# Performance work log

Hardware: AMD Instinct MI355X
Metric: run time of the kernel (lower is better)

Reference implementation:

```python
import jax, jax.numpy as jnp
import numpy as np
import math

B, S_MAX, D = 16, 4096, 4096
H, H_KV, D_H = 32, 8, 128
REP = H // H_KV
START_POS = S_MAX - 1  # decode at last slot -> attend over full cache


def _rope(t, cos, sin):
    # t: [B, 1, h, D_H]; cos/sin: [1, D_H//2] (per-position rotary factors)
    b, s, h, dh = t.shape
    tr = t.reshape(b, s, h, dh // 2, 2)
    e, o = tr[..., 0], tr[..., 1]          # even / odd components
    c = cos[None, :, None, :]              # [1, 1, 1, D_H//2]
    sn = sin[None, :, None, :]
    out = jnp.stack([e * c - o * sn, e * sn + o * c], axis=-1)
    return out.reshape(b, s, h, dh)


def setup_inputs() -> dict:
    key = jax.random.key(0)
    ks = jax.random.split(key, 8)
    x = jax.random.normal(ks[0], (B, 1, D), dtype=jnp.float32)
    cache_k = jax.random.normal(ks[1], (B, S_MAX, H_KV, D_H), dtype=jnp.float32) * 0.02
    cache_v = jax.random.normal(ks[2], (B, S_MAX, H_KV, D_H), dtype=jnp.float32) * 0.02
    wq = jax.random.normal(ks[3], (D, H * D_H), dtype=jnp.float32) * 0.02
    wk = jax.random.normal(ks[4], (D, H_KV * D_H), dtype=jnp.float32) * 0.02
    wv = jax.random.normal(ks[5], (D, H_KV * D_H), dtype=jnp.float32) * 0.02
    wo = jax.random.normal(ks[6], (H * D_H, D), dtype=jnp.float32) * 0.02
    # real RoPE angles for position START_POS
    inv_freq = 1.0 / (10000.0 ** (np.arange(0, D_H, 2, dtype=np.float32) / D_H))
    ang = np.float32(START_POS) * inv_freq  # [D_H//2]
    freqs_cos = jnp.asarray(np.cos(ang))[None, :]  # [1, 64]
    freqs_sin = jnp.asarray(np.sin(ang))[None, :]
    return {"x": x, "cache_k": cache_k, "cache_v": cache_v,
            "wq": wq, "wk": wk, "wv": wv, "wo": wo,
            "freqs_cos": freqs_cos, "freqs_sin": freqs_sin,
            "start_pos": START_POS}


def reference(x, cache_k, cache_v, wq, wk, wv, wo, freqs_cos, freqs_sin, start_pos):
    b = x.shape[0]
    xq = (x @ wq).reshape(b, 1, H, D_H)
    xk = (x @ wk).reshape(b, 1, H_KV, D_H)
    xv = (x @ wv).reshape(b, 1, H_KV, D_H)
    xq = _rope(xq, freqs_cos, freqs_sin)
    xk = _rope(xk, freqs_cos, freqs_sin)
    # KV-cache append (start_pos is a Python int -> static slice)
    cache_k = jax.lax.dynamic_update_slice(cache_k, xk, (0, start_pos, 0, 0))
    cache_v = jax.lax.dynamic_update_slice(cache_v, xv, (0, start_pos, 0, 0))
    L = start_pos + 1
    keys = cache_k[:, :L]    # [B, L, H_KV, D_H]
    # NOTE: original has `values = repeat_kv(keys, num_rep)` -- values == keys (bug),
    # reproduced faithfully here. cache_v is still written, matching the original.
    q = xq.reshape(b, 1, H_KV, REP, D_H)
    # GQA scores without materializing the repeated KV tensor
    scores = jnp.einsum('bqkrd,bskd->bkrqs', q, keys) / math.sqrt(D_H)
    attn = jax.nn.softmax(scores, axis=-1)
    out = jnp.einsum('bkrqs,bskd->bqkrd', attn, keys)  # values == keys (faithful bug)
    out = out.reshape(b, 1, H * D_H) @ wo
    return out
```

## Files before the change

kernel.cpp:

```cpp
#include <hip/hip_runtime.h>
#include <math.h>

#define BATCH 16
#define SMAX 4096
#define DMODEL 4096
#define NH 32
#define NKV 8
#define NREP 4
#define DH 128
#define QKCOLS 5120
#define NCHUNK 8
#define CHUNK 512
#define TILE 64

__global__ __launch_bounds__(256) void gemv_part(
    const float* __restrict__ in,
    const float* __restrict__ w1, int c1,
    const float* __restrict__ w2, int c2,
    float* __restrict__ part)
{
    const int tile = blockIdx.x;
    const int ch = blockIdx.y;
    const int t = threadIdx.x;
    const int col = tile * 256 + t;
    const int totC = c1 + c2;
    const int d0 = ch * 256;

    __shared__ float xs[BATCH * 256];
    for (int b = 0; b < BATCH; ++b)
        xs[b * 256 + t] = in[(size_t)b * DMODEL + d0 + t];
    __syncthreads();

    const float* w; int stride, wcol;
    if (col < c1) { w = w1; stride = c1; wcol = col; }
    else          { w = w2; stride = c2; wcol = col - c1; }

    float acc[BATCH];
#pragma unroll
    for (int b = 0; b < BATCH; ++b) acc[b] = 0.f;

    const float* wp = w + (size_t)d0 * stride + wcol;
    for (int d = 0; d < 256; d += 4) {
        float wa = wp[(size_t)(d + 0) * stride];
        float wb = wp[(size_t)(d + 1) * stride];
        float wc = wp[(size_t)(d + 2) * stride];
        float wd = wp[(size_t)(d + 3) * stride];
#pragma unroll
        for (int b = 0; b < BATCH; ++b) {
            const float4 xv = *(const float4*)&xs[b * 256 + d];
            float a = acc[b];
            a = fmaf(xv.x, wa, a);
            a = fmaf(xv.y, wb, a);
            a = fmaf(xv.z, wc, a);
            a = fmaf(xv.w, wd, a);
            acc[b] = a;
        }
    }
#pragma unroll
    for (int b = 0; b < BATCH; ++b)
        part[((size_t)ch * BATCH + b) * totC + col] = acc[b];
}

__global__ __launch_bounds__(256) void rope_reduce(
    const float* __restrict__ part,
    const float* __restrict__ fcos, const float* __restrict__ fsin,
    float* __restrict__ xqk)
{
    int g = blockIdx.x * 256 + threadIdx.x;
    int b = g / 2560;
    int po = g % 2560;
    float e = 0.f, o = 0.f;
    const float* p = part + (size_t)b * QKCOLS + 2 * po;
#pragma unroll
    for (int ch = 0; ch < 16; ++ch) {
        float2 v = *(const float2*)(p + (size_t)ch * BATCH * QKCOLS);
        e += v.x; o += v.y;
    }
    int i = po & 63;
    float c = fcos[i], s = fsin[i];
    xqk[(size_t)b * QKCOLS + 2 * po]     = e * c - o * s;
    xqk[(size_t)b * QKCOLS + 2 * po + 1] = e * s + o * c;
}

__global__ __launch_bounds__(256) void attn_part_kernel(
    const float* __restrict__ cache_k,
    const float* __restrict__ xqk,
    const int* __restrict__ sp,
    float* __restrict__ out)
{
    const int chunk = blockIdx.x;
    const int kv = blockIdx.y;
    const int b = blockIdx.z;
    const int t = threadIdx.x;
    const int dl = t & 63;
    const int r = t >> 6;
    const int start_pos = sp[0];

    __shared__ float k_lds[TILE * DH];

    const int h = kv * NREP + r;
    const float* qp = xqk + (size_t)b * QKCOLS + h * DH;
    const int half = dl & 31;
    const int hi = dl >> 5;
    float4 q4 = *(const float4*)(qp + half * 4);
    const float scale = 0.08838834764831845f;
    q4.x *= scale; q4.y *= scale; q4.z *= scale; q4.w *= scale;
    const int row_owned = (half << 1) + hi;

    const float* xknew = xqk + (size_t)b * QKCOLS + DMODEL + kv * DH;
    const float* kbase = cache_k + ((size_t)b * SMAX * NKV + kv) * DH;

    float m_run = -1e30f, l_run = 0.f;
    float2 acc = make_float2(0.f, 0.f);

    for (int tt = 0; tt < CHUNK / TILE; ++tt) {
        const int s_base = chunk * CHUNK + tt * TILE;
#pragma unroll
        for (int it = 0; it < 8; ++it) {
            int f = it * 256 + t;
            int row = f >> 5;
            int c4 = (f & 31) * 4;
            int s = s_base + row;
            const float* src = (s == start_pos) ? (xknew + c4)
                             : (kbase + (size_t)s * (NKV * DH) + c4);
            *(float4*)&k_lds[row * DH + c4] = *(const float4*)src;
        }
        __syncthreads();

        float score_mine = -1e30f;
        for (int jp = 0; jp < 32; ++jp) {
            int row = 2 * jp + hi;
            const float4 k4 = *(const float4*)&k_lds[row * DH + half * 4];
            float partial = q4.x * k4.x + q4.y * k4.y + q4.z * k4.z + q4.w * k4.w;
#pragma unroll
            for (int m = 1; m < 32; m <<= 1)
                partial += __shfl_xor(partial, m, 64);
            if (half == jp) score_mine = partial;
        }
        if (s_base + row_owned > start_pos) score_mine = -1e30f;

        float m_tile = score_mine;
#pragma unroll
        for (int m = 1; m < 64; m <<= 1)
            m_tile = fmaxf(m_tile, __shfl_xor(m_tile, m, 64));
        float m_new = fmaxf(m_run, m_tile);
        float alpha = __expf(m_run - m_new);
        float p_mine = __expf(score_mine - m_new);
        float psum = p_mine;
#pragma unroll
        for (int m = 1; m < 64; m <<= 1)
            psum += __shfl_xor(psum, m, 64);
        l_run = l_run * alpha + psum;
        acc.x *= alpha; acc.y *= alpha;
        m_run = m_new;

        for (int j = 0; j < 64; ++j) {
            int src_lane = (j >> 1) + ((j & 1) << 5);
            float pj = __shfl(p_mine, src_lane, 64);
            const float2 kj = *(const float2*)&k_lds[j * DH + 2 * dl];
            acc.x = fmaf(pj, kj.x, acc.x);
            acc.y = fmaf(pj, kj.y, acc.y);
        }
        __syncthreads();
    }

    float* rec = out + ((((size_t)b * NKV + kv) * NCHUNK + chunk) * NREP + r) * 130;
    rec[2 * dl] = acc.x;
    rec[2 * dl + 1] = acc.y;
    if (dl == 0) { rec[128] = m_run; rec[129] = l_run; }
}

__global__ __launch_bounds__(128) void attn_combine(
    const float* __restrict__ part, float* __restrict__ attn_out)
{
    const int hq = blockIdx.x;
    const int b = blockIdx.y;
    const int kv = hq >> 2, r = hq & 3;
    const int d = threadIdx.x;
    float m_c[NCHUNK], l_c[NCHUNK];
    float M = -1e30f;
#pragma unroll
    for (int c = 0; c < NCHUNK; ++c) {
        const float* rec = part + ((((size_t)b * NKV + kv) * NCHUNK + c) * NREP + r) * 130;
        m_c[c] = rec[128]; l_c[c] = rec[129];
        M = fmaxf(M, m_c[c]);
    }
    float num = 0.f, den = 0.f;
#pragma unroll
    for (int c = 0; c < NCHUNK; ++c) {
        const float* rec = part + ((((size_t)b * NKV + kv) * NCHUNK + c) * NREP + r) * 130;
        float w = __expf(m_c[c] - M);
        num = fmaf(w, rec[d], num);
        den = fmaf(w, l_c[c], den);
    }
    attn_out[(size_t)b * DMODEL + hq * DH + d] = num / den;
}

__global__ __launch_bounds__(256) void reduce_out(
    const float* __restrict__ part, float* __restrict__ out)
{
    int g = blockIdx.x * 256 + threadIdx.x;
    int b = g >> 12, o = g & 4095;
    float s = 0.f;
#pragma unroll
    for (int ch = 0; ch < 16; ++ch)
        s += part[((size_t)ch * BATCH + b) * DMODEL + o];
    out[g] = s;
}

extern "C" void kernel_launch(void* const* d_in, const int* in_sizes, int n_in,
                              void* d_out, int out_size, void* d_ws, size_t ws_size,
                              hipStream_t stream) {
    const float* x       = (const float*)d_in[0];
    const float* cache_k = (const float*)d_in[1];
    const float* wq      = (const float*)d_in[3];
    const float* wk      = (const float*)d_in[4];
    const float* wo      = (const float*)d_in[6];
    const float* fcos    = (const float*)d_in[7];
    const float* fsin    = (const float*)d_in[8];
    const int*   sp      = (const int*)d_in[9];
    float* out = (float*)d_out;
    float* ws  = (float*)d_ws;

    float* part_qk   = ws;
    float* xqk       = part_qk + 1310720;
    float* attn_part = xqk + 81920;
    float* attn_out  = attn_part + 532480;
    float* part_out  = part_qk;

    gemv_part<<<dim3(QKCOLS / 256, 16), 256, 0, stream>>>(x, wq, 4096, wk, 1024, part_qk);
    rope_reduce<<<160, 256, 0, stream>>>(part_qk, fcos, fsin, xqk);
    attn_part_kernel<<<dim3(NCHUNK, NKV, BATCH), 256, 0, stream>>>(cache_k, xqk, sp, attn_part);
    attn_combine<<<dim3(NH, BATCH), 128, 0, stream>>>(attn_part, attn_out);
    gemv_part<<<dim3(DMODEL / 256, 16), 256, 0, stream>>>(attn_out, wo, 4096, nullptr, 0, part_out);
    reduce_out<<<256, 256, 0, stream>>>(part_out, out);
}
```

Baseline: 733.2 us.

## Rework GEMV split-K and attention kernel with prefetch, swizzled LDS, per-row scores

The GEMV now has each thread own two columns via float2 loads, reads x straight from global memory instead of LDS, and splits K into 64 chunks of 64 rows for more blocks. The reductions are adjusted to match, and the workspace grows. The attention kernel is rewritten so each lane computes one full key-row score from Q held in LDS, which replaces the cross-lane shuffle reduction. It also prefetches the next K tile into registers while computing the current one, uses an XOR-swizzled LDS layout to avoid bank conflicts, and passes probabilities through LDS. The trade-off is more partial-sum traffic in the GEMV reductions, plus higher register pressure and extra barriers in attention.

```diff
diff --git a/kernel.cpp b/kernel.cpp
--- a/kernel.cpp
+++ b/kernel.cpp
@@ -12,6 +12,8 @@
 #define NCHUNK 8
 #define CHUNK 512
 #define TILE 64
+#define NCH 64
+#define GD 64
 
 __global__ __launch_bounds__(256) void gemv_part(
     const float* __restrict__ in,
@@ -19,46 +21,34 @@
     const float* __restrict__ w2, int c2,
     float* __restrict__ part)
 {
-    const int tile = blockIdx.x;
-    const int ch = blockIdx.y;
     const int t = threadIdx.x;
-    const int col = tile * 256 + t;
+    const int col = blockIdx.x * 512 + t * 2;
     const int totC = c1 + c2;
-    const int d0 = ch * 256;
-
-    __shared__ float xs[BATCH * 256];
+    const int d0 = blockIdx.y * GD;
+
+    const float* w; int stride, wc;
+    if (col < c1) { w = w1; stride = c1; wc = col; }
+    else          { w = w2; stride = c2; wc = col - c1; }
+    const float* wp = w + (size_t)d0 * stride + wc;
+
+    float2 acc[BATCH];
+#pragma unroll
+    for (int b = 0; b < BATCH; ++b) acc[b] = make_float2(0.f, 0.f);
+
+#pragma unroll 4
+    for (int i = 0; i < GD; ++i) {
+        const float2 wv = *(const float2*)(wp + (size_t)i * stride);
+#pragma unroll
+        for (int b = 0; b < BATCH; ++b) {
+            const float xv = in[(size_t)b * DMODEL + d0 + i];
+            acc[b].x = fmaf(wv.x, xv, acc[b].x);
+            acc[b].y = fmaf(wv.y, xv, acc[b].y);
+        }
+    }
+    const size_t base = (size_t)blockIdx.y * BATCH;
+#pragma unroll
     for (int b = 0; b < BATCH; ++b)
-        xs[b * 256 + t] = in[(size_t)b * DMODEL + d0 + t];
-    __syncthreads();
-
-    const float* w; int stride, wcol;
-    if (col < c1) { w = w1; stride = c1; wcol = col; }
-    else          { w = w2; stride = c2; wcol = col - c1; }
-
-    float acc[BATCH];
-#pragma unroll
-    for (int b = 0; b < BATCH; ++b) acc[b] = 0.f;
-
-    const float* wp = w + (size_t)d0 * stride + wcol;
-    for (int d = 0; d < 256; d += 4) {
-        float wa = wp[(size_t)(d + 0) * stride];
-        float wb = wp[(size_t)(d + 1) * stride];
-        float wc = wp[(size_t)(d + 2) * stride];
-        float wd = wp[(size_t)(d + 3) * stride];
-#pragma unroll
-        for (int b = 0; b < BATCH; ++b) {
-            const float4 xv = *(const float4*)&xs[b * 256 + d];
-            float a = acc[b];
-            a = fmaf(xv.x, wa, a);
-            a = fmaf(xv.y, wb, a);
-            a = fmaf(xv.z, wc, a);
-            a = fmaf(xv.w, wd, a);
-            acc[b] = a;
-        }
-    }
-#pragma unroll
-    for (int b = 0; b < BATCH; ++b)
-        part[((size_t)ch * BATCH + b) * totC + col] = acc[b];
+        *(float2*)&part[(base + b) * totC + col] = acc[b];
 }
 
 __global__ __launch_bounds__(256) void rope_reduce(
@@ -71,8 +61,8 @@
     int po = g % 2560;
     float e = 0.f, o = 0.f;
     const float* p = part + (size_t)b * QKCOLS + 2 * po;
-#pragma unroll
-    for (int ch = 0; ch < 16; ++ch) {
+#pragma unroll 8
+    for (int ch = 0; ch < NCH; ++ch) {
         float2 v = *(const float2*)(p + (size_t)ch * BATCH * QKCOLS);
         e += v.x; o += v.y;
     }
@@ -82,7 +72,7 @@
     xqk[(size_t)b * QKCOLS + 2 * po + 1] = e * s + o * c;
 }
 
-__global__ __launch_bounds__(256) void attn_part_kernel(
+__global__ __launch_bounds__(256, 4) void attn_part_kernel(
     const float* __restrict__ cache_k,
     const float* __restrict__ xqk,
     const int* __restrict__ sp,
@@ -97,77 +87,123 @@
     const int start_pos = sp[0];
 
     __shared__ float k_lds[TILE * DH];
-
-    const int h = kv * NREP + r;
-    const float* qp = xqk + (size_t)b * QKCOLS + h * DH;
-    const int half = dl & 31;
-    const int hi = dl >> 5;
-    float4 q4 = *(const float4*)(qp + half * 4);
-    const float scale = 0.08838834764831845f;
-    q4.x *= scale; q4.y *= scale; q4.z *= scale; q4.w *= scale;
-    const int row_owned = (half << 1) + hi;
+    __shared__ float q_lds[NREP * DH];
+    __shared__ float p_lds[NREP * TILE];
 
     const float* xknew = xqk + (size_t)b * QKCOLS + DMODEL + kv * DH;
     const float* kbase = cache_k + ((size_t)b * SMAX * NKV + kv) * DH;
+    const float scale = 0.08838834764831845f;
+
+    {
+        const float* qp0 = xqk + (size_t)b * QKCOLS + (kv * NREP) * DH;
+        q_lds[t]       = qp0[t] * scale;
+        q_lds[256 + t] = qp0[256 + t] * scale;
+    }
+
+    float4 st[8];
+
+#define STAGE(TT) do {                                                        \
+        const int s_b_ = chunk * CHUNK + (TT) * TILE;                         \
+        _Pragma("unroll")                                                     \
+        for (int it = 0; it < 8; ++it) {                                      \
+            int f_ = it * 256 + t;                                            \
+            int row_ = f_ >> 5;                                               \
+            int c4_ = f_ & 31;                                                \
+            int s_ = s_b_ + row_;                                             \
+            const float* src_ = (s_ == start_pos) ? (xknew + 4 * c4_)         \
+                              : (kbase + (size_t)s_ * (NKV * DH) + 4 * c4_);  \
+            st[it] = *(const float4*)src_;                                    \
+        }                                                                     \
+    } while (0)
+
+#define KWRITE() do {                                                         \
+        _Pragma("unroll")                                                     \
+        for (int it = 0; it < 8; ++it) {                                      \
+            int f_ = it * 256 + t;                                            \
+            int row_ = f_ >> 5;                                               \
+            int c4_ = f_ & 31;                                                \
+            *(float4*)&k_lds[row_ * DH + ((c4_ ^ (row_ & 7)) << 2)] = st[it]; \
+        }                                                                     \
+    } while (0)
+
+    STAGE(0);
+    KWRITE();
+    __syncthreads();
 
     float m_run = -1e30f, l_run = 0.f;
-    float2 acc = make_float2(0.f, 0.f);
+    float ax = 0.f, ay = 0.f;
+    const float* qh = q_lds + r * DH;
+    const float* krow = k_lds + dl * DH;
+    const int sw = dl & 7;
+    const int c4o = dl >> 1;
+    const int o2 = (2 * dl) & 3;
 
     for (int tt = 0; tt < CHUNK / TILE; ++tt) {
+        if (tt < CHUNK / TILE - 1) STAGE(tt + 1);
+
         const int s_base = chunk * CHUNK + tt * TILE;
-#pragma unroll
-        for (int it = 0; it < 8; ++it) {
-            int f = it * 256 + t;
-            int row = f >> 5;
-            int c4 = (f & 31) * 4;
-            int s = s_base + row;
-            const float* src = (s == start_pos) ? (xknew + c4)
-                             : (kbase + (size_t)s * (NKV * DH) + c4);
-            *(float4*)&k_lds[row * DH + c4] = *(const float4*)src;
-        }
-        __syncthreads();
-
-        float score_mine = -1e30f;
-        for (int jp = 0; jp < 32; ++jp) {
-            int row = 2 * jp + hi;
-            const float4 k4 = *(const float4*)&k_lds[row * DH + half * 4];
-            float partial = q4.x * k4.x + q4.y * k4.y + q4.z * k4.z + q4.w * k4.w;
-#pragma unroll
-            for (int m = 1; m < 32; m <<= 1)
-                partial += __shfl_xor(partial, m, 64);
-            if (half == jp) score_mine = partial;
-        }
-        if (s_base + row_owned > start_pos) score_mine = -1e30f;
-
-        float m_tile = score_mine;
+
+        float c0 = 0.f, c1 = 0.f, c2 = 0.f, c3 = 0.f;
+#pragma unroll 4
+        for (int i = 0; i < 32; ++i) {
+            const float4 q4 = *(const float4*)(qh + 4 * i);
+            const float4 k4 = *(const float4*)(krow + ((i ^ sw) << 2));
+            c0 = fmaf(q4.x, k4.x, c0);
+            c1 = fmaf(q4.y, k4.y, c1);
+            c2 = fmaf(q4.z, k4.z, c2);
+            c3 = fmaf(q4.w, k4.w, c3);
+        }
+        float score = (c0 + c1) + (c2 + c3);
+        if (s_base + dl > start_pos) score = -1e30f;
+
+        float m_tile = score;
 #pragma unroll
         for (int m = 1; m < 64; m <<= 1)
             m_tile = fmaxf(m_tile, __shfl_xor(m_tile, m, 64));
         float m_new = fmaxf(m_run, m_tile);
         float alpha = __expf(m_run - m_new);
-        float p_mine = __expf(score_mine - m_new);
-        float psum = p_mine;
+        float p = __expf(score - m_new);
+        float psum = p;
 #pragma unroll
         for (int m = 1; m < 64; m <<= 1)
             psum += __shfl_xor(psum, m, 64);
         l_run = l_run * alpha + psum;
-        acc.x *= alpha; acc.y *= alpha;
+        ax *= alpha; ay *= alpha;
         m_run = m_new;
 
-        for (int j = 0; j < 64; ++j) {
-            int src_lane = (j >> 1) + ((j & 1) << 5);
-            float pj = __shfl(p_mine, src_lane, 64);
-            const float2 kj = *(const float2*)&k_lds[j * DH + 2 * dl];
-            acc.x = fmaf(pj, kj.x, acc.x);
-            acc.y = fmaf(pj, kj.y, acc.y);
-        }
+        p_lds[r * TILE + dl] = p;
         __syncthreads();
+
+#pragma unroll 4
+        for (int j4 = 0; j4 < 16; ++j4) {
+            const float4 pj = *(const float4*)&p_lds[r * TILE + 4 * j4];
+#define PVROW(JJ, PV) do {                                                    \
+            const int rw_ = 4 * j4 + (JJ);                                    \
+            const float2 k2_ = *(const float2*)&k_lds[rw_ * DH +              \
+                                   ((c4o ^ (rw_ & 7)) << 2) + o2];            \
+            ax = fmaf((PV), k2_.x, ax);                                       \
+            ay = fmaf((PV), k2_.y, ay);                                       \
+        } while (0)
+            PVROW(0, pj.x);
+            PVROW(1, pj.y);
+            PVROW(2, pj.z);
+            PVROW(3, pj.w);
+#undef PVROW
+        }
+        __syncthreads();
+
+        if (tt < CHUNK / TILE - 1) {
+            KWRITE();
+            __syncthreads();
+        }
     }
 
     float* rec = out + ((((size_t)b * NKV + kv) * NCHUNK + chunk) * NREP + r) * 130;
-    rec[2 * dl] = acc.x;
-    rec[2 * dl + 1] = acc.y;
+    rec[2 * dl] = ax;
+    rec[2 * dl + 1] = ay;
     if (dl == 0) { rec[128] = m_run; rec[129] = l_run; }
+#undef STAGE
+#undef KWRITE
 }
 
 __global__ __launch_bounds__(128) void attn_combine(
@@ -202,8 +238,8 @@
     int g = blockIdx.x * 256 + threadIdx.x;
     int b = g >> 12, o = g & 4095;
     float s = 0.f;
-#pragma unroll
-    for (int ch = 0; ch < 16; ++ch)
+#pragma unroll 8
+    for (int ch = 0; ch < NCH; ++ch)
         s += part[((size_t)ch * BATCH + b) * DMODEL + o];
     out[g] = s;
 }
@@ -223,15 +259,15 @@
     float* ws  = (float*)d_ws;
 
     float* part_qk   = ws;
-    float* xqk       = part_qk + 1310720;
+    float* xqk       = part_qk + 5242880;
     float* attn_part = xqk + 81920;
     float* attn_out  = attn_part + 532480;
     float* part_out  = part_qk;
 
-    gemv_part<<<dim3(QKCOLS / 256, 16), 256, 0, stream>>>(x, wq, 4096, wk, 1024, part_qk);
+    gemv_part<<<dim3(QKCOLS / 512, NCH), 256, 0, stream>>>(x, wq, 4096, wk, 1024, part_qk);
     rope_reduce<<<160, 256, 0, stream>>>(part_qk, fcos, fsin, xqk);
     attn_part_kernel<<<dim3(NCHUNK, NKV, BATCH), 256, 0, stream>>>(cache_k, xqk, sp, attn_part);
     attn_combine<<<dim3(NH, BATCH), 128, 0, stream>>>(attn_part, attn_out);
-    gemv_part<<<dim3(DMODEL / 256, 16), 256, 0, stream>>>(attn_out, wo, 4096, nullptr, 0, part_out);
+    gemv_part<<<dim3(DMODEL / 512, NCH), 256, 0, stream>>>(attn_out, wo, 4096, nullptr, 0, part_out);
     reduce_out<<<256, 256, 0, stream>>>(part_out, out);
 }
```

Result: faster. 628.5 us (-14.3%).
